# Performance work log

Measured on AMD Instinct MI355X. Metric: run time of the kernel, lower is better.

## Reference

```python
import jax, jax.numpy as jnp
import numpy as np


def setup_inputs() -> dict:
    key = jax.random.key(0)
    ks = jax.random.split(key, 6)
    B, S, H, F, E = 4, 2048, 1024, 4096, 8
    x = jax.random.normal(ks[0], (B, S, H), dtype=jnp.float32)
    Wr = jax.random.normal(ks[1], (H, E), dtype=jnp.float32) * (1.0 / np.sqrt(H))
    br = jnp.zeros((E,), dtype=jnp.float32)
    W1 = jax.random.normal(ks[2], (E, H, F), dtype=jnp.float32) * (1.0 / np.sqrt(H))
    b1 = jnp.zeros((E, F), dtype=jnp.float32)
    W2 = jax.random.normal(ks[3], (E, F, H), dtype=jnp.float32) * (1.0 / np.sqrt(F))
    b2 = jnp.zeros((E, H), dtype=jnp.float32)
    b_buf = jnp.zeros((E,), dtype=jnp.float32)  # load-balancing bias buffer, zero-init
    return {"x": x, "b_buf": b_buf, "Wr": Wr, "br": br,
            "W1": W1, "b1": b1, "W2": W2, "b2": b2, "k": 2}


def reference(x, b_buf, Wr, br, W1, b1, W2, b2, k):
    # Router
    scores = jnp.einsum('bsh,he->bse', x, Wr) + br          # [B,S,E]
    probs = jax.nn.softmax(scores, axis=-1)
    # load_balancing: expert selection uses biased scores (b_buf pre-update)
    _, expert_id = jax.lax.top_k(probs + b_buf, k)          # [B,S,k] int
    # combine weights use unbiased probs
    p, _ = jax.lax.top_k(probs, k)                          # [B,S,k]
    # Dense-dispatch reference: run every expert MLP on all tokens,
    # then select via one-hot mask (same math as gather/scatter dispatch).
    h1 = jnp.einsum('bsh,ehf->ebsf', x, W1) + b1[:, None, None, :]
    h1 = jax.nn.gelu(h1, approximate=False)                 # torch nn.GELU = exact
    out_e = jnp.einsum('ebsf,efh->ebsh', h1, W2) + b2[:, None, None, :]
    E = W1.shape[0]
    onehot = (expert_id[None, :, :, :] == jnp.arange(E)[:, None, None, None]).astype(x.dtype)  # [E,B,S,k]
    out_k = jnp.einsum('ebsk,ebsh->bskh', onehot, out_e)    # scatter-combine per slot
    w = p / jnp.sum(p, axis=-1, keepdims=True)              # normalize top-k probs
    return jnp.einsum('bsk,bskh->bsh', w, out_k)
```

## Files before the change

### kernel.cpp

```cpp
#include <hip/hip_runtime.h>
#include <stdint.h>

#define NTOK 8192
#define H_ 1024
#define F_ 4096
#define E_ 8
#define VCAP 18432
#define VMBLK 72
#define NCOMP 16384

using f32x4  = __attribute__((ext_vector_type(4))) float;
using short8 = __attribute__((ext_vector_type(8))) short;

typedef __attribute__((address_space(1))) const uint32_t gu32;
typedef __attribute__((address_space(3))) uint32_t lu32;

__device__ __forceinline__ void glds16(const void* g, void* l) {
  __builtin_amdgcn_global_load_lds((gu32*)g, (lu32*)l, 16, 0, 0);
}

__device__ __forceinline__ ushort f2bf(float f) {
  union { float f; uint32_t u; } v; v.f = f;
  uint32_t r = (v.u + 0x7FFFu + ((v.u >> 16) & 1u)) >> 16;
  return (ushort)r;
}

__device__ __forceinline__ float gelu_t(float x) {
  float u = 0.7978845608028654f * (x + 0.044715f * x * x * x);
  float e = exp2f(u * 2.885390081777927f);
  float th = 1.0f - 2.0f / (1.0f + e);
  return 0.5f * x * (1.0f + th);
}

__global__ void k_init(int* cnt, int* cur, int* tok, float* wl, int* v2c) {
  int i = blockIdx.x * 256 + threadIdx.x;
  if (i < E_) { cnt[i] = 0; cur[i] = 0; }
  if (i < VCAP) { tok[i] = -1; wl[i] = 0.f; v2c[i] = -1; }
}

__global__ __launch_bounds__(256) void k_transcvt(const float* __restrict__ W,
                                                  ushort* __restrict__ WT,
                                                  int R, int C) {
  __shared__ float t[64][65];
  int e = blockIdx.z;
  int c0 = blockIdx.x * 64, r0 = blockIdx.y * 64;
  const float* Wp = W + (size_t)e * R * C;
  ushort* Tp = WT + (size_t)e * R * C;
  int tx = threadIdx.x & 15, ty = threadIdx.x >> 4;
#pragma unroll
  for (int i = 0; i < 4; i++) {
    int lr = ty + i * 16;
    const float4 v = *(const float4*)&Wp[(size_t)(r0 + lr) * C + c0 + tx * 4];
    t[lr][tx * 4 + 0] = v.x; t[lr][tx * 4 + 1] = v.y;
    t[lr][tx * 4 + 2] = v.z; t[lr][tx * 4 + 3] = v.w;
  }
  __syncthreads();
#pragma unroll
  for (int i = 0; i < 4; i++) {
    int lc = ty + i * 16;
    ushort4 o;
    o.x = f2bf(t[tx * 4 + 0][lc]);
    o.y = f2bf(t[tx * 4 + 1][lc]);
    o.z = f2bf(t[tx * 4 + 2][lc]);
    o.w = f2bf(t[tx * 4 + 3][lc]);
    *(ushort4*)&Tp[(size_t)(c0 + lc) * R + r0 + tx * 4] = o;
  }
}

__global__ __launch_bounds__(256) void k_router(const float* __restrict__ x,
                                                const float* __restrict__ Wr,
                                                const float* __restrict__ br,
                                                const float* __restrict__ bbuf,
                                                int* cnt, int* te, float* tw) {
  int wid = threadIdx.x >> 6, lane = threadIdx.x & 63;
  int t = blockIdx.x * 4 + wid;
  const float* xp = x + (size_t)t * H_;
  double acc[E_];
#pragma unroll
  for (int e = 0; e < E_; e++) acc[e] = 0.0;
  for (int j = lane; j < H_; j += 64) {
    float xv = xp[j];
    const float4 w0 = *(const float4*)&Wr[j * 8];
    const float4 w1 = *(const float4*)&Wr[j * 8 + 4];
    acc[0] += (double)xv * (double)w0.x;
    acc[1] += (double)xv * (double)w0.y;
    acc[2] += (double)xv * (double)w0.z;
    acc[3] += (double)xv * (double)w0.w;
    acc[4] += (double)xv * (double)w1.x;
    acc[5] += (double)xv * (double)w1.y;
    acc[6] += (double)xv * (double)w1.z;
    acc[7] += (double)xv * (double)w1.w;
  }
#pragma unroll
  for (int e = 0; e < E_; e++)
    for (int s = 32; s > 0; s >>= 1) acc[e] += __shfl_xor(acc[e], s);
  if (lane == 0) {
    double s[E_], m = -1e300;
    for (int e = 0; e < E_; e++) { s[e] = acc[e] + (double)br[e]; if (s[e] > m) m = s[e]; }
    double pe[E_], sum = 0.0;
    for (int e = 0; e < E_; e++) { pe[e] = exp(s[e] - m); sum += pe[e]; }
    double pr[E_], bb[E_];
    for (int e = 0; e < E_; e++) { pr[e] = pe[e] / sum; bb[e] = pr[e] + (double)bbuf[e]; }
    int e0 = 0;
    for (int e = 1; e < E_; e++) if (bb[e] > bb[e0]) e0 = e;
    int e1 = (e0 == 0) ? 1 : 0;
    for (int e = 0; e < E_; e++) if (e != e0 && bb[e] > bb[e1]) e1 = e;
    int a0 = 0;
    for (int e = 1; e < E_; e++) if (pr[e] > pr[a0]) a0 = e;
    int a1 = (a0 == 0) ? 1 : 0;
    for (int e = 0; e < E_; e++) if (e != a0 && pr[e] > pr[a1]) a1 = e;
    double iv = 1.0 / (pr[a0] + pr[a1]);
    te[t * 2] = e0; te[t * 2 + 1] = e1;
    tw[t * 2] = (float)(pr[a0] * iv); tw[t * 2 + 1] = (float)(pr[a1] * iv);
    atomicAdd(&cnt[e0], 1); atomicAdd(&cnt[e1], 1);
  }
}

__global__ void k_offsets(const int* cnt, int* off, int* coff) {
  if (threadIdx.x == 0 && blockIdx.x == 0) {
    int o = 0, c = 0;
    for (int e = 0; e < E_; e++) {
      off[e] = o; coff[e] = c;
      o += ((cnt[e] + 255) >> 8) << 8;
      c += cnt[e];
    }
    off[E_] = o; coff[E_] = c;
  }
}

__global__ void k_build(const int* __restrict__ te, const float* __restrict__ tw,
                        const int* __restrict__ off, const int* __restrict__ coff,
                        int* cur, int* tok, float* wl, int* v2c, int* ctok) {
  int t = blockIdx.x * 256 + threadIdx.x;
  if (t >= NTOK) return;
#pragma unroll
  for (int s = 0; s < 2; s++) {
    int e = te[t * 2 + s];
    int slot = atomicAdd(&cur[e], 1);
    int vp = off[e] + slot;
    int cp = coff[e] + slot;
    tok[vp] = t; wl[vp] = tw[t * 2 + s]; v2c[vp] = cp; ctok[cp] = t;
  }
}

__global__ __launch_bounds__(256) void k_gather(const float* __restrict__ x,
                                                const int* __restrict__ ctok,
                                                ushort* __restrict__ Xg) {
  int row = blockIdx.x;
  int t = ctok[row];
  const float4* src = (const float4*)(x + (size_t)t * H_);
  ushort4* dst = (ushort4*)(Xg + (size_t)row * H_);
  int i = threadIdx.x;
  float4 v = src[i];
  ushort4 o; o.x = f2bf(v.x); o.y = f2bf(v.y); o.z = f2bf(v.z); o.w = f2bf(v.w);
  dst[i] = o;
}

__global__ void k_zero(float* out) {
  size_t i = (size_t)blockIdx.x * 256 + threadIdx.x;
  float4 z; z.x = 0.f; z.y = 0.f; z.z = 0.f; z.w = 0.f;
  ((float4*)out)[i] = z;
}

template <int MODE>
__global__ __launch_bounds__(512) void k_gemm(const ushort* __restrict__ A,
                                              const ushort* __restrict__ BT,
                                              const float* __restrict__ bias,
                                              ushort* __restrict__ h1,
                                              float* __restrict__ Out,
                                              const int* __restrict__ off,
                                              const int* __restrict__ v2c,
                                              const int* __restrict__ tok,
                                              const float* __restrict__ wl,
                                              int K, int N, int NTe) {
  extern __shared__ char lds[];
  int nwg = gridDim.x;
  int cpx = nwg >> 3;
  int bid = blockIdx.x;
  int lid = (bid & 7) * cpx + (bid >> 3);
  int gsz = NTe << 2;
  int g = lid / gsz, rm = lid % gsz;
  int ne = rm >> 2, m = (g << 2) + (rm & 3);
  int row0 = m << 8;
  if (row0 >= off[E_]) return;
  int e = 0;
  while (off[e + 1] <= row0) e++;
  int n0, k0, nk;
  if (MODE == 0) { n0 = ne << 8; k0 = 0; nk = K >> 6; }
  else           { n0 = (ne >> 1) << 8; k0 = (ne & 1) * (K >> 1); nk = K >> 7; }
  const ushort* Bp = BT + (size_t)e * (size_t)N * (size_t)K;

  int tid = threadIdx.x, lane = tid & 63, w = tid >> 6;
  int wr = w >> 2, wc = w & 3;

  f32x4 acc[8][4];
#pragma unroll
  for (int mm = 0; mm < 8; mm++)
#pragma unroll
    for (int nn = 0; nn < 4; nn++) acc[mm][nn] = (f32x4){0.f, 0.f, 0.f, 0.f};

  int urow = (w << 3) + (lane >> 3);
  int schunk = (lane & 7) ^ (lane >> 3);
  const char *aS0, *aS1, *aS2, *aS3, *bS0, *bS1, *bS2, *bS3;
  {
    int v0 = v2c[row0 + 0 * 64 + urow];   if (v0 < 0) v0 = 0;
    int v1 = v2c[row0 + 1 * 64 + urow];   if (v1 < 0) v1 = 0;
    int v2 = v2c[row0 + 2 * 64 + urow];   if (v2 < 0) v2 = 0;
    int v3 = v2c[row0 + 3 * 64 + urow];   if (v3 < 0) v3 = 0;
    size_t kb = (size_t)k0 * 2 + (size_t)schunk * 16;
    aS0 = (const char*)(A + (size_t)v0 * K) + kb;
    aS1 = (const char*)(A + (size_t)v1 * K) + kb;
    aS2 = (const char*)(A + (size_t)v2 * K) + kb;
    aS3 = (const char*)(A + (size_t)v3 * K) + kb;
    bS0 = (const char*)(Bp + (size_t)(n0 + 0 * 64 + urow) * K) + kb;
    bS1 = (const char*)(Bp + (size_t)(n0 + 1 * 64 + urow) * K) + kb;
    bS2 = (const char*)(Bp + (size_t)(n0 + 2 * 64 + urow) * K) + kb;
    bS3 = (const char*)(Bp + (size_t)(n0 + 3 * 64 + urow) * K) + kb;
  }

  int fr = lane & 15, fq = lane >> 4;
  int frs = fr & 7;

  short8 af_[4][2], bf_[2][2];

#define STG_A(u, tt, bbuf) glds16(aS##u + (size_t)(tt) * 128, lds + (bbuf) * 65536 + (u) * 8192 + (w << 10))
#define STG_B(u, tt, bbuf) glds16(bS##u + (size_t)(tt) * 128, lds + (bbuf) * 65536 + 32768 + (u) * 8192 + (w << 10))

#define RDA(mmq, bbuf) do {                                                  \
    const ushort* LA_ = (const ushort*)(lds + (bbuf) * 65536);               \
    _Pragma("unroll")                                                        \
    for (int i = 0; i < 4; ++i)                                              \
      _Pragma("unroll")                                                      \
      for (int ks = 0; ks < 2; ++ks)                                         \
        af_[i][ks] = *(const short8*)&LA_[((wr << 7) + ((mmq) + i) * 16 + fr) * 64 + (((ks << 2) + fq) ^ frs) * 8]; \
  } while (0)

#define RDB(nnq, bbuf) do {                                                  \
    const ushort* LB_ = (const ushort*)(lds + (bbuf) * 65536 + 32768);       \
    _Pragma("unroll")                                                        \
    for (int i = 0; i < 2; ++i)                                              \
      _Pragma("unroll")                                                      \
      for (int ks = 0; ks < 2; ++ks)                                         \
        bf_[i][ks] = *(const short8*)&LB_[((wc << 6) + ((nnq) + i) * 16 + fr) * 64 + (((ks << 2) + fq) ^ frs) * 8]; \
  } while (0)

#define MMQ(mmq, nnq) do {                                                   \
    __builtin_amdgcn_s_setprio(1);                                           \
    _Pragma("unroll")                                                        \
    for (int i = 0; i < 4; ++i)                                              \
      _Pragma("unroll")                                                      \
      for (int jn = 0; jn < 2; ++jn)                                         \
        _Pragma("unroll")                                                    \
        for (int ks = 0; ks < 2; ++ks)                                       \
          acc[(mmq) + i][(nnq) + jn] = __builtin_amdgcn_mfma_f32_16x16x32_bf16(af_[i][ks], bf_[jn][ks], acc[(mmq) + i][(nnq) + jn], 0, 0, 0); \
    __builtin_amdgcn_s_setprio(0);                                           \
  } while (0)

#define FENCE() __builtin_amdgcn_sched_barrier(0)
#define BAR()   __builtin_amdgcn_s_barrier()

  STG_B(0, 0, 0); STG_B(1, 0, 0); STG_B(2, 0, 0); STG_B(3, 0, 0);
  STG_A(0, 0, 0); STG_A(2, 0, 0); STG_A(1, 0, 0); STG_A(3, 0, 0);
  asm volatile("s_waitcnt vmcnt(2)" ::: "memory");
  BAR(); FENCE();

  for (int t = 0; t < nk; ++t) {
    int bb = t & 1, nb = bb ^ 1;
    bool pre = (t + 1 < nk);
    if (pre) { STG_B(0, t + 1, nb); STG_B(1, t + 1, nb); }
    RDB(0, bb); RDA(0, bb);
    MMQ(0, 0);
    FENCE();
    if (pre) asm volatile("s_waitcnt vmcnt(2)" ::: "memory");
    else     asm volatile("s_waitcnt vmcnt(0)" ::: "memory");
    BAR(); FENCE();
    if (pre) { STG_B(2, t + 1, nb); STG_B(3, t + 1, nb); }
    RDA(4, bb);
    MMQ(4, 0);
    FENCE(); BAR(); FENCE();
    if (pre) { STG_A(0, t + 1, nb); STG_A(2, t + 1, nb); }
    RDB(2, bb);
    MMQ(4, 2);
    FENCE(); BAR(); FENCE();
    if (pre) { STG_A(1, t + 1, nb); STG_A(3, t + 1, nb); }
    RDA(0, bb);
    MMQ(0, 2);
    FENCE();
    if (pre) asm volatile("s_waitcnt vmcnt(2)" ::: "memory");
    BAR(); FENCE();
  }
#undef STG_A
#undef STG_B
#undef RDA
#undef RDB
#undef MMQ
#undef FENCE
#undef BAR

  const float* bp = bias + (size_t)e * N;
  int cb = n0 + (wc << 6);
  if (MODE == 0) {
#pragma unroll
    for (int mm = 0; mm < 8; mm++) {
#pragma unroll
      for (int j = 0; j < 4; j++) {
        int vr = row0 + (wr << 7) + mm * 16 + (fq << 2) + j;
        int cr = v2c[vr];
        if (cr < 0) continue;
        ushort* hp = h1 + (size_t)cr * N + cb;
#pragma unroll
        for (int nn = 0; nn < 4; nn++) {
          float v = acc[mm][nn][j] + bp[cb + nn * 16 + fr];
          hp[nn * 16 + fr] = f2bf(gelu_t(v));
        }
      }
    }
  } else {
    bool addb = (k0 == 0);
#pragma unroll
    for (int mm = 0; mm < 8; mm++) {
#pragma unroll
      for (int j = 0; j < 4; j++) {
        int vr = row0 + (wr << 7) + mm * 16 + (fq << 2) + j;
        int t2 = tok[vr];
        if (t2 < 0) continue;
        float wgt = wl[vr];
#pragma unroll
        for (int nn = 0; nn < 4; nn++) {
          int c = cb + nn * 16 + fr;
          float v = acc[mm][nn][j] + (addb ? bp[c] : 0.f);
          atomicAdd(&Out[(size_t)t2 * (size_t)N + c], wgt * v);
        }
      }
    }
  }
}

extern "C" void kernel_launch(void* const* d_in, const int* in_sizes, int n_in,
                              void* d_out, int out_size, void* d_ws, size_t ws_size,
                              hipStream_t stream) {
  (void)in_sizes; (void)n_in; (void)out_size; (void)ws_size;
  const float* x    = (const float*)d_in[0];
  const float* bbuf = (const float*)d_in[1];
  const float* Wr   = (const float*)d_in[2];
  const float* br   = (const float*)d_in[3];
  const float* W1   = (const float*)d_in[4];
  const float* b1   = (const float*)d_in[5];
  const float* W2   = (const float*)d_in[6];
  const float* b2   = (const float*)d_in[7];
  float* out = (float*)d_out;

  char* ws = (char*)d_ws;
  ushort* W1T = (ushort*)ws;
  ushort* W2T = (ushort*)(ws + 67108864);
  ushort* Xg  = (ushort*)(ws + 134217728);
  ushort* h1  = (ushort*)(ws + 167772160);
  char* meta  = ws + 301989888;
  int*   cnt  = (int*)(meta);
  int*   off  = (int*)(meta + 64);
  int*   coff = (int*)(meta + 128);
  int*   cur  = (int*)(meta + 192);
  int*   te   = (int*)(meta + 256);
  float* tw   = (float*)(meta + 65792);
  int*   tok  = (int*)(meta + 131328);
  float* wl   = (float*)(meta + 205056);
  int*   v2c  = (int*)(meta + 278784);
  int*   ctok = (int*)(meta + 352512);

  hipFuncSetAttribute((const void*)&k_gemm<0>,
                      hipFuncAttributeMaxDynamicSharedMemorySize, 131072);
  hipFuncSetAttribute((const void*)&k_gemm<1>,
                      hipFuncAttributeMaxDynamicSharedMemorySize, 131072);

  k_init<<<VMBLK, 256, 0, stream>>>(cnt, cur, tok, wl, v2c);
  k_transcvt<<<dim3(F_ / 64, H_ / 64, E_), 256, 0, stream>>>(W1, W1T, H_, F_);
  k_transcvt<<<dim3(H_ / 64, F_ / 64, E_), 256, 0, stream>>>(W2, W2T, F_, H_);
  k_router<<<NTOK / 4, 256, 0, stream>>>(x, Wr, br, bbuf, cnt, te, tw);
  k_offsets<<<1, 64, 0, stream>>>(cnt, off, coff);
  k_build<<<NTOK / 256, 256, 0, stream>>>(te, tw, off, coff, cur, tok, wl, v2c, ctok);
  k_gather<<<NCOMP, 256, 0, stream>>>(x, ctok, Xg);
  k_zero<<<(NTOK * H_ / 4) / 256, 256, 0, stream>>>(out);
  k_gemm<0><<<16 * VMBLK, 512, 131072, stream>>>(Xg, W1T, b1, h1, nullptr,
                                                 off, v2c, nullptr, nullptr,
                                                 H_, F_, 16);
  k_gemm<1><<<8 * VMBLK, 512, 131072, stream>>>(h1, W2T, b2, nullptr, out,
                                                off, v2c, tok, wl,
                                                F_, H_, 8);
}
```

Before: 1.004 ms.

## Fuse prep kernels, merge zeroing into gather, and restructure GEMM pipeline

Merges the router, metadata init and both weight transpose-convert passes into one launch, and makes each transpose block handle four 64-wide tiles. Output zeroing moves into the gather kernel and counters are cleared with a memset, which cuts kernel launches. The GEMM main loop is reordered so each half-iteration stages all of B or all of A for the next step, with full vmcnt(0) and lgkmcnt waits. The block-to-tile mapping is simplified to row-major over VMBLK. The stricter waits and extra barriers may expose more load latency inside the GEMM.

```diff
diff --git a/kernel.cpp b/kernel.cpp
--- a/kernel.cpp
+++ b/kernel.cpp
@@ -32,88 +32,116 @@
   return 0.5f * x * (1.0f + th);
 }
 
-__global__ void k_init(int* cnt, int* cur, int* tok, float* wl, int* v2c) {
-  int i = blockIdx.x * 256 + threadIdx.x;
-  if (i < E_) { cnt[i] = 0; cur[i] = 0; }
-  if (i < VCAP) { tok[i] = -1; wl[i] = 0.f; v2c[i] = -1; }
-}
-
-__global__ __launch_bounds__(256) void k_transcvt(const float* __restrict__ W,
-                                                  ushort* __restrict__ WT,
-                                                  int R, int C) {
-  __shared__ float t[64][65];
-  int e = blockIdx.z;
-  int c0 = blockIdx.x * 64, r0 = blockIdx.y * 64;
+__device__ __forceinline__ void transcvt_tile4(const float* __restrict__ W,
+                                               ushort* __restrict__ WT,
+                                               int R, int C, int t4,
+                                               float (*tb)[65]) {
+  int nxw = C >> 8;
+  int per_e = (R >> 6) * nxw;
+  int e = t4 / per_e, rem = t4 % per_e;
+  int r0 = (rem / nxw) << 6, c0 = (rem % nxw) << 8;
   const float* Wp = W + (size_t)e * R * C;
   ushort* Tp = WT + (size_t)e * R * C;
   int tx = threadIdx.x & 15, ty = threadIdx.x >> 4;
-#pragma unroll
-  for (int i = 0; i < 4; i++) {
-    int lr = ty + i * 16;
-    const float4 v = *(const float4*)&Wp[(size_t)(r0 + lr) * C + c0 + tx * 4];
-    t[lr][tx * 4 + 0] = v.x; t[lr][tx * 4 + 1] = v.y;
-    t[lr][tx * 4 + 2] = v.z; t[lr][tx * 4 + 3] = v.w;
-  }
-  __syncthreads();
-#pragma unroll
-  for (int i = 0; i < 4; i++) {
-    int lc = ty + i * 16;
-    ushort4 o;
-    o.x = f2bf(t[tx * 4 + 0][lc]);
-    o.y = f2bf(t[tx * 4 + 1][lc]);
-    o.z = f2bf(t[tx * 4 + 2][lc]);
-    o.w = f2bf(t[tx * 4 + 3][lc]);
-    *(ushort4*)&Tp[(size_t)(c0 + lc) * R + r0 + tx * 4] = o;
-  }
-}
-
-__global__ __launch_bounds__(256) void k_router(const float* __restrict__ x,
-                                                const float* __restrict__ Wr,
-                                                const float* __restrict__ br,
-                                                const float* __restrict__ bbuf,
-                                                int* cnt, int* te, float* tw) {
-  int wid = threadIdx.x >> 6, lane = threadIdx.x & 63;
-  int t = blockIdx.x * 4 + wid;
-  const float* xp = x + (size_t)t * H_;
-  double acc[E_];
-#pragma unroll
-  for (int e = 0; e < E_; e++) acc[e] = 0.0;
-  for (int j = lane; j < H_; j += 64) {
-    float xv = xp[j];
-    const float4 w0 = *(const float4*)&Wr[j * 8];
-    const float4 w1 = *(const float4*)&Wr[j * 8 + 4];
-    acc[0] += (double)xv * (double)w0.x;
-    acc[1] += (double)xv * (double)w0.y;
-    acc[2] += (double)xv * (double)w0.z;
-    acc[3] += (double)xv * (double)w0.w;
-    acc[4] += (double)xv * (double)w1.x;
-    acc[5] += (double)xv * (double)w1.y;
-    acc[6] += (double)xv * (double)w1.z;
-    acc[7] += (double)xv * (double)w1.w;
-  }
-#pragma unroll
-  for (int e = 0; e < E_; e++)
-    for (int s = 32; s > 0; s >>= 1) acc[e] += __shfl_xor(acc[e], s);
-  if (lane == 0) {
-    double s[E_], m = -1e300;
-    for (int e = 0; e < E_; e++) { s[e] = acc[e] + (double)br[e]; if (s[e] > m) m = s[e]; }
-    double pe[E_], sum = 0.0;
-    for (int e = 0; e < E_; e++) { pe[e] = exp(s[e] - m); sum += pe[e]; }
-    double pr[E_], bb[E_];
-    for (int e = 0; e < E_; e++) { pr[e] = pe[e] / sum; bb[e] = pr[e] + (double)bbuf[e]; }
-    int e0 = 0;
-    for (int e = 1; e < E_; e++) if (bb[e] > bb[e0]) e0 = e;
-    int e1 = (e0 == 0) ? 1 : 0;
-    for (int e = 0; e < E_; e++) if (e != e0 && bb[e] > bb[e1]) e1 = e;
-    int a0 = 0;
-    for (int e = 1; e < E_; e++) if (pr[e] > pr[a0]) a0 = e;
-    int a1 = (a0 == 0) ? 1 : 0;
-    for (int e = 0; e < E_; e++) if (e != a0 && pr[e] > pr[a1]) a1 = e;
-    double iv = 1.0 / (pr[a0] + pr[a1]);
-    te[t * 2] = e0; te[t * 2 + 1] = e1;
-    tw[t * 2] = (float)(pr[a0] * iv); tw[t * 2 + 1] = (float)(pr[a1] * iv);
-    atomicAdd(&cnt[e0], 1); atomicAdd(&cnt[e1], 1);
-  }
+
+  float4 v[4][4];
+#pragma unroll
+  for (int p = 0; p < 4; p++)
+#pragma unroll
+    for (int i = 0; i < 4; i++) {
+      int lr = ty + i * 16;
+      v[p][i] = *(const float4*)&Wp[(size_t)(r0 + lr) * C + c0 + p * 64 + tx * 4];
+    }
+#pragma unroll
+  for (int p = 0; p < 4; p++) {
+    __syncthreads();
+#pragma unroll
+    for (int i = 0; i < 4; i++) {
+      int lr = ty + i * 16;
+      tb[lr][tx * 4 + 0] = v[p][i].x; tb[lr][tx * 4 + 1] = v[p][i].y;
+      tb[lr][tx * 4 + 2] = v[p][i].z; tb[lr][tx * 4 + 3] = v[p][i].w;
+    }
+    __syncthreads();
+#pragma unroll
+    for (int i = 0; i < 4; i++) {
+      int lc = ty + i * 16;
+      ushort4 o;
+      o.x = f2bf(tb[tx * 4 + 0][lc]);
+      o.y = f2bf(tb[tx * 4 + 1][lc]);
+      o.z = f2bf(tb[tx * 4 + 2][lc]);
+      o.w = f2bf(tb[tx * 4 + 3][lc]);
+      *(ushort4*)&Tp[(size_t)(c0 + p * 64 + lc) * R + r0 + tx * 4] = o;
+    }
+  }
+}
+
+__global__ __launch_bounds__(256) void k_prep2(const float* __restrict__ W1,
+                                               ushort* __restrict__ W1T,
+                                               const float* __restrict__ W2,
+                                               ushort* __restrict__ W2T,
+                                               const float* __restrict__ x,
+                                               const float* __restrict__ Wr,
+                                               const float* __restrict__ br,
+                                               const float* __restrict__ bbuf,
+                                               int* cnt, int* te, float* tw,
+                                               int* tok, float* wl, int* v2c) {
+  __shared__ float tb[64][65];
+  int bid = blockIdx.x;
+  if (bid < 2048) {
+    int wid = threadIdx.x >> 6, lane = threadIdx.x & 63;
+    int t = bid * 4 + wid;
+    const float* xp = x + (size_t)t * H_;
+    double acc[E_];
+#pragma unroll
+    for (int e = 0; e < E_; e++) acc[e] = 0.0;
+    for (int j = lane; j < H_; j += 64) {
+      float xv = xp[j];
+      const float4 w0 = *(const float4*)&Wr[j * 8];
+      const float4 w1 = *(const float4*)&Wr[j * 8 + 4];
+      acc[0] += (double)xv * (double)w0.x;
+      acc[1] += (double)xv * (double)w0.y;
+      acc[2] += (double)xv * (double)w0.z;
+      acc[3] += (double)xv * (double)w0.w;
+      acc[4] += (double)xv * (double)w1.x;
+      acc[5] += (double)xv * (double)w1.y;
+      acc[6] += (double)xv * (double)w1.z;
+      acc[7] += (double)xv * (double)w1.w;
+    }
+#pragma unroll
+    for (int e = 0; e < E_; e++)
+      for (int s = 32; s > 0; s >>= 1) acc[e] += __shfl_xor(acc[e], s);
+    if (lane == 0) {
+      double s[E_], m = -1e300;
+      for (int e = 0; e < E_; e++) { s[e] = acc[e] + (double)br[e]; if (s[e] > m) m = s[e]; }
+      double pe[E_], sum = 0.0;
+      for (int e = 0; e < E_; e++) { pe[e] = exp(s[e] - m); sum += pe[e]; }
+      double pr[E_], bb[E_];
+      for (int e = 0; e < E_; e++) { pr[e] = pe[e] / sum; bb[e] = pr[e] + (double)bbuf[e]; }
+      int e0 = 0;
+      for (int e = 1; e < E_; e++) if (bb[e] > bb[e0]) e0 = e;
+      int e1 = (e0 == 0) ? 1 : 0;
+      for (int e = 0; e < E_; e++) if (e != e0 && bb[e] > bb[e1]) e1 = e;
+      int a0 = 0;
+      for (int e = 1; e < E_; e++) if (pr[e] > pr[a0]) a0 = e;
+      int a1 = (a0 == 0) ? 1 : 0;
+      for (int e = 0; e < E_; e++) if (e != a0 && pr[e] > pr[a1]) a1 = e;
+      double iv = 1.0 / (pr[a0] + pr[a1]);
+      te[t * 2] = e0; te[t * 2 + 1] = e1;
+      tw[t * 2] = (float)(pr[a0] * iv); tw[t * 2 + 1] = (float)(pr[a1] * iv);
+      atomicAdd(&cnt[e0], 1); atomicAdd(&cnt[e1], 1);
+    }
+    return;
+  }
+  if (bid < 4096) {
+    int tcb = bid - 2048;
+    if (tcb < VMBLK) {
+      int i = tcb * 256 + threadIdx.x;
+      if (i < VCAP) { tok[i] = -1; wl[i] = 0.f; v2c[i] = -1; }
+    }
+    transcvt_tile4(W1, W1T, 1024, 4096, tcb, tb);
+    return;
+  }
+  transcvt_tile4(W2, W2T, 4096, 1024, bid - 4096, tb);
 }
 
 __global__ void k_offsets(const int* cnt, int* off, int* coff) {
@@ -145,7 +173,13 @@
 
 __global__ __launch_bounds__(256) void k_gather(const float* __restrict__ x,
                                                 const int* __restrict__ ctok,
-                                                ushort* __restrict__ Xg) {
+                                                ushort* __restrict__ Xg,
+                                                float* __restrict__ out) {
+  int gid = blockIdx.x * 256 + threadIdx.x;
+  if (gid < NTOK * H_ / 4) {
+    float4 z; z.x = 0.f; z.y = 0.f; z.z = 0.f; z.w = 0.f;
+    ((float4*)out)[gid] = z;
+  }
   int row = blockIdx.x;
   int t = ctok[row];
   const float4* src = (const float4*)(x + (size_t)t * H_);
@@ -154,12 +188,6 @@
   float4 v = src[i];
   ushort4 o; o.x = f2bf(v.x); o.y = f2bf(v.y); o.z = f2bf(v.z); o.w = f2bf(v.w);
   dst[i] = o;
-}
-
-__global__ void k_zero(float* out) {
-  size_t i = (size_t)blockIdx.x * 256 + threadIdx.x;
-  float4 z; z.x = 0.f; z.y = 0.f; z.z = 0.f; z.w = 0.f;
-  ((float4*)out)[i] = z;
 }
 
 template <int MODE>
@@ -172,22 +200,20 @@
                                               const int* __restrict__ v2c,
                                               const int* __restrict__ tok,
                                               const float* __restrict__ wl,
-                                              int K, int N, int NTe) {
+                                              int K, int N) {
   extern __shared__ char lds[];
   int nwg = gridDim.x;
   int cpx = nwg >> 3;
   int bid = blockIdx.x;
   int lid = (bid & 7) * cpx + (bid >> 3);
-  int gsz = NTe << 2;
-  int g = lid / gsz, rm = lid % gsz;
-  int ne = rm >> 2, m = (g << 2) + (rm & 3);
+  int ne = lid / VMBLK, m = lid % VMBLK;
   int row0 = m << 8;
   if (row0 >= off[E_]) return;
   int e = 0;
   while (off[e + 1] <= row0) e++;
   int n0, k0, nk;
   if (MODE == 0) { n0 = ne << 8; k0 = 0; nk = K >> 6; }
-  else           { n0 = (ne >> 1) << 8; k0 = (ne & 1) * (K >> 1); nk = K >> 7; }
+  else           { n0 = (ne & 3) << 8; k0 = (ne >> 2) * (K >> 1); nk = K >> 7; }
   const ushort* Bp = BT + (size_t)e * (size_t)N * (size_t)K;
 
   int tid = threadIdx.x, lane = tid & 63, w = tid >> 6;
@@ -258,35 +284,38 @@
 
 #define FENCE() __builtin_amdgcn_sched_barrier(0)
 #define BAR()   __builtin_amdgcn_s_barrier()
+#define WLGKM() asm volatile("s_waitcnt lgkmcnt(0)" ::: "memory")
+#define WVM0()  asm volatile("s_waitcnt vmcnt(0)" ::: "memory")
 
   STG_B(0, 0, 0); STG_B(1, 0, 0); STG_B(2, 0, 0); STG_B(3, 0, 0);
-  STG_A(0, 0, 0); STG_A(2, 0, 0); STG_A(1, 0, 0); STG_A(3, 0, 0);
-  asm volatile("s_waitcnt vmcnt(2)" ::: "memory");
+  STG_A(0, 0, 0); STG_A(1, 0, 0); STG_A(2, 0, 0); STG_A(3, 0, 0);
+  WVM0();
   BAR(); FENCE();
 
-  for (int t = 0; t < nk; ++t) {
-    int bb = t & 1, nb = bb ^ 1;
-    bool pre = (t + 1 < nk);
-    if (pre) { STG_B(0, t + 1, nb); STG_B(1, t + 1, nb); }
-    RDB(0, bb); RDA(0, bb);
+  for (int T = 0; T < nk; ++T) {
+    int b = T & 1, nb = b ^ 1;
+    bool pre = (T + 1 < nk);
+    RDA(0, b); RDB(0, b);
+    if (pre) { STG_B(0, T + 1, nb); STG_B(1, T + 1, nb);
+               STG_B(2, T + 1, nb); STG_B(3, T + 1, nb); }
+    BAR(); WLGKM(); FENCE();
     MMQ(0, 0);
-    FENCE();
-    if (pre) asm volatile("s_waitcnt vmcnt(2)" ::: "memory");
-    else     asm volatile("s_waitcnt vmcnt(0)" ::: "memory");
-    BAR(); FENCE();
-    if (pre) { STG_B(2, t + 1, nb); STG_B(3, t + 1, nb); }
-    RDA(4, bb);
+    BAR();
+    RDA(4, b);
+    if (pre) { STG_A(0, T + 1, nb); STG_A(1, T + 1, nb);
+               STG_A(2, T + 1, nb); STG_A(3, T + 1, nb); }
+    BAR(); WLGKM(); FENCE();
     MMQ(4, 0);
-    FENCE(); BAR(); FENCE();
-    if (pre) { STG_A(0, t + 1, nb); STG_A(2, t + 1, nb); }
-    RDB(2, bb);
+    BAR();
+    RDB(2, b);
+    BAR(); WLGKM(); FENCE();
     MMQ(4, 2);
-    FENCE(); BAR(); FENCE();
-    if (pre) { STG_A(1, t + 1, nb); STG_A(3, t + 1, nb); }
-    RDA(0, bb);
+    BAR();
+    RDA(0, b);
+    BAR(); WLGKM(); FENCE();
     MMQ(0, 2);
     FENCE();
-    if (pre) asm volatile("s_waitcnt vmcnt(2)" ::: "memory");
+    if (pre) WVM0();
     BAR(); FENCE();
   }
 #undef STG_A
@@ -296,6 +325,8 @@
 #undef MMQ
 #undef FENCE
 #undef BAR
+#undef WLGKM
+#undef WVM0
 
   const float* bp = bias + (size_t)e * N;
   int cb = n0 + (wc << 6);
@@ -372,18 +403,17 @@
   hipFuncSetAttribute((const void*)&k_gemm<1>,
                       hipFuncAttributeMaxDynamicSharedMemorySize, 131072);
 
-  k_init<<<VMBLK, 256, 0, stream>>>(cnt, cur, tok, wl, v2c);
-  k_transcvt<<<dim3(F_ / 64, H_ / 64, E_), 256, 0, stream>>>(W1, W1T, H_, F_);
-  k_transcvt<<<dim3(H_ / 64, F_ / 64, E_), 256, 0, stream>>>(W2, W2T, F_, H_);
-  k_router<<<NTOK / 4, 256, 0, stream>>>(x, Wr, br, bbuf, cnt, te, tw);
+  hipMemsetAsync(meta, 0, 256, stream);
+
+  k_prep2<<<6144, 256, 0, stream>>>(W1, W1T, W2, W2T, x, Wr, br, bbuf,
+                                    cnt, te, tw, tok, wl, v2c);
   k_offsets<<<1, 64, 0, stream>>>(cnt, off, coff);
   k_build<<<NTOK / 256, 256, 0, stream>>>(te, tw, off, coff, cur, tok, wl, v2c, ctok);
-  k_gather<<<NCOMP, 256, 0, stream>>>(x, ctok, Xg);
-  k_zero<<<(NTOK * H_ / 4) / 256, 256, 0, stream>>>(out);
+  k_gather<<<NCOMP, 256, 0, stream>>>(x, ctok, Xg, out);
   k_gemm<0><<<16 * VMBLK, 512, 131072, stream>>>(Xg, W1T, b1, h1, nullptr,
                                                  off, v2c, nullptr, nullptr,
-                                                 H_, F_, 16);
+                                                 H_, F_);
   k_gemm<1><<<8 * VMBLK, 512, 131072, stream>>>(h1, W2T, b2, nullptr, out,
                                                 off, v2c, tok, wl,
-                                                F_, H_, 8);
-}
+                                                F_, H_);
+}
```

New measurement: 968.8 us. 1.04x faster.
